# Kernel tuning notes

Hardware: AMD Instinct MI355X
Metric: run time of the kernel (lower is better)

## Reference

```python
import jax, jax.numpy as jnp
import numpy as np

N_PAPER, N_AUTHOR = 200000, 100000
D_PAPER, D_AUTHOR = 128, 64
H, OUT = 64, 32
E_CITES, E_WRITES = 4000000, 2000000


def _gcn(x, W, b, src, dst, n):
    # GCNConv with default add_self_loops=True, symmetric normalization
    xl = x @ W
    deg = jnp.zeros((n,), xl.dtype).at[dst].add(1.0) + 1.0  # +1 for self loop
    dis = jax.lax.rsqrt(deg)
    norm = dis[src] * dis[dst]
    out = jax.ops.segment_sum(xl[src] * norm[:, None], dst, num_segments=n)
    out = out + xl * (dis * dis)[:, None]  # self-loop term: norm_ii = 1/deg_i
    return out + b


def _sage(x_src, x_dst, Wl, bl, Wr, src, dst, n_dst):
    # SAGEConv: mean neighbor aggregation -> lin_l, plus root lin_r on dst
    ones = jnp.ones(src.shape, x_src.dtype)
    cnt = jnp.maximum(jax.ops.segment_sum(ones, dst, num_segments=n_dst), 1.0)
    mean = jax.ops.segment_sum(x_src[src], dst, num_segments=n_dst) / cnt[:, None]
    return mean @ Wl + bl + x_dst @ Wr


def _gat(x_src, x_dst, Ws, Wd, a_s, a_d, b, src, dst, n_dst):
    # GATConv heads=1, bipartite, add_self_loops=False, leaky_relu slope 0.2
    xs = x_src @ Ws  # [Ns, H]
    xd = x_dst @ Wd  # [Nd, H]
    a_src = xs @ a_s  # [Ns]
    a_dst = xd @ a_d  # [Nd]
    e = a_src[src] + a_dst[dst]
    e = jnp.where(e > 0, e, 0.2 * e)
    m = jax.ops.segment_max(e, dst, num_segments=n_dst)
    m = jnp.where(jnp.isfinite(m), m, 0.0)  # nodes with no in-edges
    ex = jnp.exp(e - m[dst])
    denom = jax.ops.segment_sum(ex, dst, num_segments=n_dst)
    alpha = ex / denom[dst]
    out = jax.ops.segment_sum(alpha[:, None] * xs[src], dst, num_segments=n_dst)
    return out + b


def _forward(x_paper, x_author, params, cites_src, cites_dst, writes_src, writes_dst):
    for (gW, gb, sWl, sbl, sWr, aWs, aWd, aas, aad, ab) in params:
        p_gcn = _gcn(x_paper, gW, gb, cites_src, cites_dst, N_PAPER)
        p_sage = _sage(x_author, x_paper, sWl, sbl, sWr, writes_src, writes_dst, N_PAPER)
        # rev_writes: paper -> author, i.e. src=writes_dst (paper), dst=writes_src (author)
        a_gat = _gat(x_paper, x_author, aWs, aWd, aas, aad, ab, writes_dst, writes_src, N_AUTHOR)
        x_paper = jax.nn.relu(p_gcn + p_sage)  # HeteroConv aggr='sum'
        x_author = jax.nn.relu(a_gat)
    return x_paper, x_author


def setup_inputs() -> dict:
    key = jax.random.key(0)
    ks = jax.random.split(key, 40)
    rn = lambda i, shp, s=0.1: jax.random.normal(ks[i], shp, jnp.float32) * s
    inp = {}
    inp['x_paper'] = rn(0, (N_PAPER, D_PAPER), 1.0)
    inp['x_author'] = rn(1, (N_AUTHOR, D_AUTHOR), 1.0)
    dims = [(D_PAPER, D_AUTHOR), (H, H)]
    i = 2
    for l, (dp, da) in enumerate(dims):
        inp[f'gcn_W{l}'] = rn(i, (dp, H)); i += 1
        inp[f'gcn_b{l}'] = jnp.zeros((H,), jnp.float32)
        inp[f'sage_Wl{l}'] = rn(i, (da, H)); i += 1
        inp[f'sage_bl{l}'] = jnp.zeros((H,), jnp.float32)
        inp[f'sage_Wr{l}'] = rn(i, (dp, H)); i += 1
        inp[f'gat_Ws{l}'] = rn(i, (dp, H)); i += 1
        inp[f'gat_Wd{l}'] = rn(i, (da, H)); i += 1
        inp[f'gat_as{l}'] = rn(i, (H,)); i += 1
        inp[f'gat_ad{l}'] = rn(i, (H,)); i += 1
        inp[f'gat_b{l}'] = jnp.zeros((H,), jnp.float32)
    inp['lin_W'] = rn(i, (H, OUT)); i += 1
    inp['lin_b'] = jnp.zeros((OUT,), jnp.float32)
    inp['cites_src'] = jax.random.randint(ks[30], (E_CITES,), 0, N_PAPER)
    inp['cites_dst'] = jax.random.randint(ks[31], (E_CITES,), 0, N_PAPER)
    inp['writes_src'] = jax.random.randint(ks[32], (E_WRITES,), 0, N_AUTHOR)
    inp['writes_dst'] = jax.random.randint(ks[33], (E_WRITES,), 0, N_PAPER)
    return inp


def reference(x_paper, x_author,
              gcn_W0, gcn_b0, sage_Wl0, sage_bl0, sage_Wr0,
              gat_Ws0, gat_Wd0, gat_as0, gat_ad0, gat_b0,
              gcn_W1, gcn_b1, sage_Wl1, sage_bl1, sage_Wr1,
              gat_Ws1, gat_Wd1, gat_as1, gat_ad1, gat_b1,
              lin_W, lin_b,
              cites_src, cites_dst, writes_src, writes_dst):
    params = [
        (gcn_W0, gcn_b0, sage_Wl0, sage_bl0, sage_Wr0, gat_Ws0, gat_Wd0, gat_as0, gat_ad0, gat_b0),
        (gcn_W1, gcn_b1, sage_Wl1, sage_bl1, sage_Wr1, gat_Ws1, gat_Wd1, gat_as1, gat_ad1, gat_b1),
    ]
    _, x_author_out = _forward(x_paper, x_author, params, cites_src, cites_dst, writes_src, writes_dst)
    return x_author_out @ lin_W + lin_b
```

## Files before the change

kernel.cpp:

```cpp
#include <hip/hip_runtime.h>
#include <hip/hip_bf16.h>

#define NP 200000
#define NA 100000
#define DP 128
#define HD 64
#define EC 4000000
#define EW 2000000
#define NSCAN (2 * NP + NA)
#define NBUCK 4
#define CAPC 64
#define CAPW 48
#define CAPA 64

typedef __hip_bfloat16 bf16;
typedef __attribute__((ext_vector_type(8))) short short8;
typedef __attribute__((ext_vector_type(4))) float f32x4;

__device__ __forceinline__ float bf2f(bf16 h) { return __bfloat162float(h); }

__device__ __forceinline__ short8 pack8(float4 a, float4 b) {
    union {
        short8 s;
        unsigned u[4];
    } r;
    __hip_bfloat162 h;
    h = __float22bfloat162_rn(float2{a.x, a.y});
    r.u[0] = *reinterpret_cast<unsigned*>(&h);
    h = __float22bfloat162_rn(float2{a.z, a.w});
    r.u[1] = *reinterpret_cast<unsigned*>(&h);
    h = __float22bfloat162_rn(float2{b.x, b.y});
    r.u[2] = *reinterpret_cast<unsigned*>(&h);
    h = __float22bfloat162_rn(float2{b.z, b.w});
    r.u[3] = *reinterpret_cast<unsigned*>(&h);
    return r.s;
}


__global__ __launch_bounds__(256) void fill_pass_kernel(const int* __restrict__ cs,
                                                        const int* __restrict__ cd,
                                                        const int* __restrict__ ws,
                                                        const int* __restrict__ wd,
                                                        int* __restrict__ CUR,
                                                        int* __restrict__ colC,
                                                        int* __restrict__ colWd,
                                                        int* __restrict__ colWa, int bucket) {
    long i = (long)blockIdx.x * 256 + threadIdx.x;
    if (i < EC) {
        int d = __builtin_nontemporal_load(&cd[i]);
        if ((int)(((long)d * NBUCK) / NP) != bucket) return;
        int s = __builtin_nontemporal_load(&cs[i]);
        int pos = atomicAdd(&CUR[d * 4], 1);
        if (pos < CAPC) colC[(size_t)d * CAPC + pos] = s;
    } else if (i < (long)EC + EW) {
        long e = i - EC;
        int d = __builtin_nontemporal_load(&wd[e]);
        int a = __builtin_nontemporal_load(&ws[e]);
        if ((int)(((long)d * NBUCK) / NP) == bucket) {
            int pos = atomicAdd(&CUR[(NP + d) * 4], 1);
            if (pos < CAPW) colWd[(size_t)d * CAPW + pos] = a;
        }
        if ((int)(((long)a * NBUCK) / NA) == bucket) {
            int pos = atomicAdd(&CUR[(2 * NP + a) * 4], 1);
            if (pos < CAPA) colWa[(size_t)a * CAPA + pos] = d;
        }
    }
}


__global__ __launch_bounds__(256) void conv_author_kernel(const float* __restrict__ XA,
                                                          const float* __restrict__ wvec,
                                                          bf16* __restrict__ XAbf,
                                                          float* __restrict__ adst) {
    __shared__ float vs[64];
    if (threadIdx.x < 64) vs[threadIdx.x] = wvec[threadIdx.x];
    __syncthreads();
    int r = blockIdx.x * 4 + (threadIdx.x >> 6);
    int lane = threadIdx.x & 63;
    float x = XA[(size_t)r * 64 + lane];
    XAbf[(size_t)r * 64 + lane] = __float2bfloat16(x);
    float p = x * vs[lane];
#pragma unroll
    for (int o = 32; o > 0; o >>= 1) p += __shfl_xor(p, o, 64);
    if (lane == 0) adst[r] = p;
}


__global__ void wprep_kernel(const float* __restrict__ Wg, const float* __restrict__ Wl,
                             const float* __restrict__ Wr, const float* __restrict__ Ws0,
                             const float* __restrict__ Ws1, short* __restrict__ WF,
                             const float* __restrict__ Wd0, const float* __restrict__ ad0,
                             const float* __restrict__ Wd1, const float* __restrict__ ad1,
                             float* __restrict__ wvec0, float* __restrict__ wvec1) {
    int bid = blockIdx.x;
    int lane = threadIdx.x;
    if (bid >= 64) {
        const float* Wd = (bid == 64) ? Wd0 : Wd1;
        const float* ad = (bid == 64) ? ad0 : ad1;
        float* wv = (bid == 64) ? wvec0 : wvec1;
        float s = 0.f;
        for (int c = 0; c < 64; c++) s += Wd[lane * 64 + c] * ad[c];
        wv[lane] = s;
        return;
    }
    int q = lane & 15, g = lane >> 4;
    int m, r;
    size_t dst;
    if (bid < 16) {
        m = 0; r = bid; dst = 0;
    } else if (bid < 40) {
        m = 1; r = bid - 16; dst = 8192;
    } else if (bid < 56) {
        m = 2; r = bid - 40; dst = 20480;
    } else {
        m = 3; r = bid - 56; dst = 28672;
    }
    int ks = r >> 2, n = r & 3;
    int col = n * 16 + q;
    float v[8];
#pragma unroll
    for (int j = 0; j < 8; j++) {
        int kr = ks * 32 + g * 8 + j;
        float x;
        if (m == 0) x = Wg[(size_t)kr * 64 + col];
        else if (m == 1) x = (kr < 64) ? Wl[(size_t)kr * 64 + col] : Wr[(size_t)(kr - 64) * 64 + col];
        else if (m == 2) x = Ws0[(size_t)kr * 64 + col];
        else x = Ws1[(size_t)kr * 64 + col];
        v[j] = x;
    }
    short8 s = pack8(float4{v[0], v[1], v[2], v[3]}, float4{v[4], v[5], v[6], v[7]});
    *reinterpret_cast<short8*>(WF + dst + ((size_t)r * 64 + lane) * 8) = s;
}


__global__ __launch_bounds__(256) void fused2_gemm_kernel(const float* __restrict__ XP,
                                                          const short* __restrict__ WFg,
                                                          const short* __restrict__ WFs,
                                                          bf16* __restrict__ BF,
                                                          bf16* __restrict__ XS0,
                                                          const float* __restrict__ avec,
                                                          float* __restrict__ adot,
                                                          const int* __restrict__ CURs) {
    int tid = threadIdx.x;
    int lane = tid & 63, q = lane & 15, g = lane >> 4;
    int rw = blockIdx.x * 64 + (tid >> 6) * 16;
    int arow = rw + q;
    f32x4 accg[4], accs[4];
#pragma unroll
    for (int n = 0; n < 4; n++) {
        accg[n] = f32x4{0.f, 0.f, 0.f, 0.f};
        accs[n] = f32x4{0.f, 0.f, 0.f, 0.f};
    }
#pragma unroll
    for (int ks = 0; ks < 4; ks++) {
        const float* xr = XP + (size_t)arow * DP + ks * 32 + g * 8;
        float4 a0 = *reinterpret_cast<const float4*>(xr);
        float4 a1 = *reinterpret_cast<const float4*>(xr + 4);
        short8 af = pack8(a0, a1);
#pragma unroll
        for (int n = 0; n < 4; n++) {
            short8 bg = *reinterpret_cast<const short8*>(WFg + ((size_t)(ks * 4 + n) * 64 + lane) * 8);
            accg[n] = __builtin_amdgcn_mfma_f32_16x16x32_bf16(af, bg, accg[n], 0, 0, 0);
        }
#pragma unroll
        for (int n = 0; n < 4; n++) {
            short8 bs = *reinterpret_cast<const short8*>(WFs + ((size_t)(ks * 4 + n) * 64 + lane) * 8);
            accs[n] = __builtin_amdgcn_mfma_f32_16x16x32_bf16(af, bs, accs[n], 0, 0, 0);
        }
    }
    float av[4];
#pragma unroll
    for (int n = 0; n < 4; n++) av[n] = avec[n * 16 + q];
#pragma unroll
    for (int j = 0; j < 4; j++) {
        int R = rw + g * 4 + j;
        float sc = rsqrtf((float)CURs[(unsigned)R * 4] + 1.0f);
#pragma unroll
        for (int n = 0; n < 4; n++) {
            BF[(size_t)R * 64 + n * 16 + q] = __float2bfloat16(accg[n][j] * sc);
            XS0[(size_t)R * 64 + n * 16 + q] = __float2bfloat16(accs[n][j]);
        }
        float t = accs[0][j] * av[0] + accs[1][j] * av[1] + accs[2][j] * av[2] + accs[3][j] * av[3];
        t += __shfl_xor(t, 1, 64);
        t += __shfl_xor(t, 2, 64);
        t += __shfl_xor(t, 4, 64);
        t += __shfl_xor(t, 8, 64);
        if (q == 0) adot[R] = t;
    }
}


template <int K, int ASTRIDE, bool ABF16, bool ADOT, bool SCALE>
__global__ __launch_bounds__(256) void mfma_gemm_kernel(const void* __restrict__ Xv,
                                                        const short* __restrict__ Wf,
                                                        bf16* __restrict__ outb,
                                                        const float* __restrict__ avec,
                                                        float* __restrict__ adot,
                                                        const int* __restrict__ CURs) {
    int tid = threadIdx.x;
    int lane = tid & 63, q = lane & 15, g = lane >> 4;
    int rw = blockIdx.x * 64 + (tid >> 6) * 16;
    int arow = rw + q;
    f32x4 acc[4];
#pragma unroll
    for (int n = 0; n < 4; n++) acc[n] = f32x4{0.f, 0.f, 0.f, 0.f};
#pragma unroll
    for (int ks = 0; ks < K / 32; ks++) {
        short8 af;
        if constexpr (ABF16) {
            af = *reinterpret_cast<const short8*>((const bf16*)Xv + (size_t)arow * ASTRIDE +
                                                  ks * 32 + g * 8);
        } else {
            const float* xr = (const float*)Xv + (size_t)arow * ASTRIDE + ks * 32 + g * 8;
            float4 a0 = *reinterpret_cast<const float4*>(xr);
            float4 a1 = *reinterpret_cast<const float4*>(xr + 4);
            af = pack8(a0, a1);
        }
#pragma unroll
        for (int n = 0; n < 4; n++) {
            short8 bfr =
                *reinterpret_cast<const short8*>(Wf + ((size_t)(ks * 4 + n) * 64 + lane) * 8);
            acc[n] = __builtin_amdgcn_mfma_f32_16x16x32_bf16(af, bfr, acc[n], 0, 0, 0);
        }
    }
    float av[4];
    if constexpr (ADOT) {
#pragma unroll
        for (int n = 0; n < 4; n++) av[n] = avec[n * 16 + q];
    }
#pragma unroll
    for (int j = 0; j < 4; j++) {
        int R = rw + g * 4 + j;
        float sc = 1.f;
        if constexpr (SCALE) sc = rsqrtf((float)CURs[(unsigned)R * 4] + 1.0f);
#pragma unroll
        for (int n = 0; n < 4; n++) {
            outb[(size_t)R * 64 + n * 16 + q] = __float2bfloat16(acc[n][j] * sc);
        }
        if constexpr (ADOT) {
            float t = acc[0][j] * av[0] + acc[1][j] * av[1] + acc[2][j] * av[2] + acc[3][j] * av[3];
            t += __shfl_xor(t, 1, 64);
            t += __shfl_xor(t, 2, 64);
            t += __shfl_xor(t, 4, 64);
            t += __shfl_xor(t, 8, 64);
            if (q == 0) adot[R] = t;
        }
    }
}


__global__ __launch_bounds__(256) void mfma_sage_kernel(const bf16* B3s,
                                                        const float* __restrict__ XP,
                                                        const float* __restrict__ B2,
                                                        const float* __restrict__ bl,
                                                        const short* __restrict__ Wf, bf16* P1) {
    int tid = threadIdx.x;
    int lane = tid & 63, q = lane & 15, g = lane >> 4;
    int rw = blockIdx.x * 64 + (tid >> 6) * 16;
    int arow = rw + q;
    f32x4 acc[4];
#pragma unroll
    for (int n = 0; n < 4; n++) acc[n] = f32x4{0.f, 0.f, 0.f, 0.f};
#pragma unroll
    for (int ks = 0; ks < 6; ks++) {
        short8 af;
        if (ks < 2) {
            af = *reinterpret_cast<const short8*>(B3s + (size_t)arow * 128 + 64 + ks * 32 + g * 8);
        } else {
            const float* xr = XP + (size_t)arow * DP + (ks - 2) * 32 + g * 8;
            float4 a0 = *reinterpret_cast<const float4*>(xr);
            float4 a1 = *reinterpret_cast<const float4*>(xr + 4);
            af = pack8(a0, a1);
        }
#pragma unroll
        for (int n = 0; n < 4; n++) {
            short8 bfr =
                *reinterpret_cast<const short8*>(Wf + ((size_t)(ks * 4 + n) * 64 + lane) * 8);
            acc[n] = __builtin_amdgcn_mfma_f32_16x16x32_bf16(af, bfr, acc[n], 0, 0, 0);
        }
    }
    float blv[4];
#pragma unroll
    for (int n = 0; n < 4; n++) blv[n] = bl[n * 16 + q];
#pragma unroll
    for (int j = 0; j < 4; j++) {
        int R = rw + g * 4 + j;
#pragma unroll
        for (int n = 0; n < 4; n++) {
            int col = n * 16 + q;
            float v = acc[n][j] + B2[(size_t)R * 64 + col] + blv[n];
            P1[(size_t)R * 128 + col] = __float2bfloat16(fmaxf(v, 0.f));
        }
    }
}


__global__ __launch_bounds__(256) void paper_gather_kernel(const bf16* __restrict__ B1,
                                                           const bf16* __restrict__ XA,
                                                           const int* __restrict__ CUR,
                                                           const int* colC,
                                                           const int* __restrict__ colWd,
                                                           const float* __restrict__ gb,
                                                           float* __restrict__ B2, bf16* B3s) {
    int node = __builtin_amdgcn_readfirstlane(blockIdx.x * 4 + (threadIdx.x >> 6));
    unsigned lane = threadIdx.x & 63;
    int degc_t = CUR[(unsigned)node * 4];
    float dd = rsqrtf((float)degc_t + 1.0f);
    int degc = min(degc_t, CAPC);
    unsigned cb = (unsigned)node * CAPC;
    float acc = bf2f(B1[((unsigned)node << 6) + lane]);
    int e = 0;
    for (; e + 8 <= degc; e += 8) {
        unsigned off[8];
#pragma unroll
        for (int j = 0; j < 8; j++) off[j] = ((unsigned)colC[cb + e + j] << 6) + lane;
        float v[8];
#pragma unroll
        for (int j = 0; j < 8; j++) v[j] = bf2f(B1[off[j]]);
#pragma unroll
        for (int j = 0; j < 8; j++) acc += v[j];
    }
    for (; e + 4 <= degc; e += 4) {
        unsigned o0 = ((unsigned)colC[cb + e] << 6) + lane;
        unsigned o1 = ((unsigned)colC[cb + e + 1] << 6) + lane;
        unsigned o2 = ((unsigned)colC[cb + e + 2] << 6) + lane;
        unsigned o3 = ((unsigned)colC[cb + e + 3] << 6) + lane;
        float v0 = bf2f(B1[o0]), v1 = bf2f(B1[o1]);
        float v2 = bf2f(B1[o2]), v3 = bf2f(B1[o3]);
        acc += v0 + v1;
        acc += v2 + v3;
    }
    for (; e < degc; e++) acc += bf2f(B1[((unsigned)colC[cb + e] << 6) + lane]);
    B2[((unsigned)node << 6) + lane] = acc * dd + gb[lane];
    int degw_t = CUR[((unsigned)NP + node) * 4];
    float ic = 1.0f / fmaxf((float)degw_t, 1.0f);
    int degw = min(degw_t, CAPW);
    unsigned wb = (unsigned)node * CAPW;
    float s = 0.f;
    e = 0;
    for (; e + 8 <= degw; e += 8) {
        unsigned off[8];
#pragma unroll
        for (int j = 0; j < 8; j++) off[j] = ((unsigned)colWd[wb + e + j] << 6) + lane;
        float v[8];
#pragma unroll
        for (int j = 0; j < 8; j++) v[j] = bf2f(XA[off[j]]);
#pragma unroll
        for (int j = 0; j < 8; j++) s += v[j];
    }
    for (; e + 4 <= degw; e += 4) {
        unsigned o0 = ((unsigned)colWd[wb + e] << 6) + lane;
        unsigned o1 = ((unsigned)colWd[wb + e + 1] << 6) + lane;
        unsigned o2 = ((unsigned)colWd[wb + e + 2] << 6) + lane;
        unsigned o3 = ((unsigned)colWd[wb + e + 3] << 6) + lane;
        float v0 = bf2f(XA[o0]), v1 = bf2f(XA[o1]);
        float v2 = bf2f(XA[o2]), v3 = bf2f(XA[o3]);
        s += v0 + v1;
        s += v2 + v3;
    }
    for (; e < degw; e++) s += bf2f(XA[((unsigned)colWd[wb + e] << 6) + lane]);
    B3s[(unsigned)node * 128u + 64u + lane] = __float2bfloat16(s * ic);
}


__device__ __forceinline__ float lrelu(float v) { return v > 0.f ? v : 0.2f * v; }

__device__ __forceinline__ void gat_phase(const bf16* __restrict__ XS, const int2* pxl, int deg,
                                          unsigned lane, float& accO) {
    float acc = 0.f;
    int l = 0;
    for (; l + 8 <= deg; l += 8) {
        float v[8], x[8];
#pragma unroll
        for (int j = 0; j < 8; j++) {
            int2 px = pxl[l + j];
            x[j] = __int_as_float(px.y);
            v[j] = bf2f(XS[((unsigned)px.x << 6) + lane]);
        }
#pragma unroll
        for (int j = 0; j < 8; j++) acc += x[j] * v[j];
    }
    for (; l < deg; l++) {
        int2 px = pxl[l];
        acc += __int_as_float(px.y) * bf2f(XS[((unsigned)px.x << 6) + lane]);
    }
    accO = acc;
}

__global__ __launch_bounds__(256) void gat_fused_kernel(
    const bf16* __restrict__ XS0, const bf16* __restrict__ XS1, const int* __restrict__ CUR,
    const int* __restrict__ colA, const float* __restrict__ asrc0,
    const float* __restrict__ asrc1, const float* __restrict__ adst0,
    const float* __restrict__ ab0, const float* __restrict__ wvec1,
    const float* __restrict__ ab1, const float* __restrict__ linW,
    const float* __restrict__ linb, float* __restrict__ out) {
    __shared__ float Ws[64 * 32];
    __shared__ float vbuf[4][64];
    __shared__ float lbs[32];
    __shared__ int2 pxlds[4][64];
    int tid = threadIdx.x;
    for (int i = tid; i < 64 * 32; i += 256) Ws[i] = linW[i];
    if (tid < 32) lbs[tid] = linb[tid];
    __syncthreads();
    int wid = tid >> 6;
    int a = __builtin_amdgcn_readfirstlane(blockIdx.x * 4 + wid);
    unsigned lane = tid & 63;
    int deg = min(CUR[(2u * NP + a) * 4], CAPA);
    unsigned cb = (unsigned)a * CAPA;
    int pi = (lane < (unsigned)deg) ? colA[cb + lane] : 0;
    bool act = lane < (unsigned)deg;
    float x0 = act ? __expf(lrelu(asrc0[(unsigned)pi] + adst0[(unsigned)a])) : 0.f;
    float den0 = x0;
#pragma unroll
    for (int o = 32; o > 0; o >>= 1) den0 += __shfl_xor(den0, o, 64);
    pxlds[wid][lane] = int2{pi, __float_as_int(x0)};
    float acc0;
    gat_phase(XS0, pxlds[wid], deg, lane, acc0);
    float inv0 = den0 > 0.f ? 1.f / den0 : 0.f;
    float val0 = fmaxf(acc0 * inv0 + ab0[lane], 0.f);
    float ada1 = val0 * wvec1[lane];
#pragma unroll
    for (int o = 32; o > 0; o >>= 1) ada1 += __shfl_xor(ada1, o, 64);
    float x1 = act ? __expf(lrelu(asrc1[(unsigned)pi] + ada1)) : 0.f;
    float den1 = x1;
#pragma unroll
    for (int o = 32; o > 0; o >>= 1) den1 += __shfl_xor(den1, o, 64);
    pxlds[wid][lane] = int2{pi, __float_as_int(x1)};
    float acc1;
    gat_phase(XS1, pxlds[wid], deg, lane, acc1);
    float inv1 = den1 > 0.f ? 1.f / den1 : 0.f;
    vbuf[wid][lane] = fmaxf(acc1 * inv1 + ab1[lane], 0.f);
    __syncthreads();
    if (tid < 128) {
        int w = tid >> 5, c = tid & 31;
        int node = blockIdx.x * 4 + w;
        float s = lbs[c];
#pragma unroll
        for (int k = 0; k < 64; k++) s += vbuf[w][k] * Ws[k * 32 + c];
        out[(size_t)node * 32 + c] = s;
    }
}


static inline int cdivi(long a, long b) { return (int)((a + b - 1) / b); }

extern "C" void kernel_launch(void* const* d_in, const int* in_sizes, int n_in, void* d_out,
                              int out_size, void* d_ws, size_t ws_size, hipStream_t stream) {
    const float* x_paper = (const float*)d_in[0];
    const float* x_author = (const float*)d_in[1];
    const float* gcn_W0 = (const float*)d_in[2];
    const float* gcn_b0 = (const float*)d_in[3];
    const float* sage_Wl0 = (const float*)d_in[4];
    const float* sage_bl0 = (const float*)d_in[5];
    const float* sage_Wr0 = (const float*)d_in[6];
    const float* gat_Ws0 = (const float*)d_in[7];
    const float* gat_Wd0 = (const float*)d_in[8];
    const float* gat_as0 = (const float*)d_in[9];
    const float* gat_ad0 = (const float*)d_in[10];
    const float* gat_b0 = (const float*)d_in[11];
    const float* gat_Ws1 = (const float*)d_in[17];
    const float* gat_Wd1 = (const float*)d_in[18];
    const float* gat_as1 = (const float*)d_in[19];
    const float* gat_ad1 = (const float*)d_in[20];
    const float* gat_b1 = (const float*)d_in[21];
    const float* lin_W = (const float*)d_in[22];
    const float* lin_b = (const float*)d_in[23];
    const int* cites_src = (const int*)d_in[24];
    const int* cites_dst = (const int*)d_in[25];
    const int* writes_src = (const int*)d_in[26];
    const int* writes_dst = (const int*)d_in[27];

    float* out = (float*)d_out;

    char* base = (char*)d_ws;
    bf16* BF = (bf16*)base;
    base += (size_t)NP * 64 * 2;
    float* B2 = (float*)base;
    base += (size_t)NP * 64 * 4;
    int* colC = (int*)base;
    bf16* R3 = (bf16*)base;
    base += (size_t)NP * CAPC * 4;
    int* colWd = (int*)base;
    bf16* XS1 = (bf16*)base;
    base += (size_t)NP * CAPW * 4;
    int* colWa = (int*)base;
    base += (size_t)NA * CAPA * 4;
    bf16* XAbf = (bf16*)base;
    base += (size_t)NA * 64 * 2;
    bf16* XS0 = (bf16*)base;
    base += (size_t)NP * 64 * 2;
    int* CUR = (int*)base;
    base += (size_t)NSCAN * 4 * 4;
    float* asrc0 = (float*)base;
    float* asrc1 = asrc0 + NP;
    float* adst0 = asrc1 + NP;
    float* wvec0 = adst0 + NA;
    float* wvec1 = wvec0 + 64;
    short* WF = (short*)(wvec1 + 64);

    dim3 blk(256);
    const long EMERGED = (long)EC + EW;

    hipMemsetAsync(CUR, 0, (size_t)NSCAN * 4 * 4, stream);
    wprep_kernel<<<66, 64, 0, stream>>>(gcn_W0, sage_Wl0, sage_Wr0, gat_Ws0, gat_Ws1, WF, gat_Wd0,
                                        gat_ad0, gat_Wd1, gat_ad1, wvec0, wvec1);

    for (int b = 0; b < NBUCK; b++) {
        fill_pass_kernel<<<cdivi(EMERGED, 256), blk, 0, stream>>>(cites_src, cites_dst,
                                                                  writes_src, writes_dst, CUR,
                                                                  colC, colWd, colWa, b);
    }

    conv_author_kernel<<<NA / 4, blk, 0, stream>>>(x_author, wvec0, XAbf, adst0);

    fused2_gemm_kernel<<<NP / 64, blk, 0, stream>>>(x_paper, WF, WF + 20480, BF, XS0, gat_as0,
                                                    asrc0, CUR);

    paper_gather_kernel<<<NP / 4, blk, 0, stream>>>(BF, XAbf, CUR, colC, colWd, gcn_b0, B2, R3);

    mfma_sage_kernel<<<NP / 64, blk, 0, stream>>>(R3, x_paper, B2, sage_bl0, WF + 8192, R3);

    mfma_gemm_kernel<HD, 128, true, true, false><<<NP / 64, blk, 0, stream>>>(
        R3, WF + 28672, XS1, gat_as1, asrc1, nullptr);

    gat_fused_kernel<<<NA / 4, blk, 0, stream>>>(XS0, XS1, CUR, colWa, asrc0, asrc1, adst0,
                                                 gat_b0, wvec1, gat_b1, lin_W, lin_b, out);
}
```

Measured before the change: 792.2 us.

## Fuse SAGE epilogue with layer-1 GAT projection and widen gather unrolls

Merges the SAGE GEMM and the following layer-1 GAT source projection into one kernel. The relu'd paper features stay in LDS and feed a second MFMA, so the intermediate bf16 tensor is never written to or read back from global memory, and one launch is removed. It also adds a 16-wide unrolled edge loop to the paper gather, and makes the GAT phase read its (index, weight) pairs as int4 with 16-wide unrolling to raise memory-level parallelism. The price is higher register pressure and an extra block barrier in the fused kernel.

```diff
diff --git a/kernel.cpp b/kernel.cpp
--- a/kernel.cpp
+++ b/kernel.cpp
@@ -190,73 +190,20 @@
 }
 
 
-template <int K, int ASTRIDE, bool ABF16, bool ADOT, bool SCALE>
-__global__ __launch_bounds__(256) void mfma_gemm_kernel(const void* __restrict__ Xv,
-                                                        const short* __restrict__ Wf,
-                                                        bf16* __restrict__ outb,
-                                                        const float* __restrict__ avec,
-                                                        float* __restrict__ adot,
-                                                        const int* __restrict__ CURs) {
+__global__ __launch_bounds__(256) void sage_l1_kernel(const bf16* __restrict__ B3s,
+                                                      const float* __restrict__ XP,
+                                                      const float* __restrict__ B2,
+                                                      const float* __restrict__ bl,
+                                                      const short* __restrict__ WfS,
+                                                      const short* __restrict__ Wf1,
+                                                      bf16* __restrict__ XS1,
+                                                      const float* __restrict__ avec,
+                                                      float* __restrict__ adot) {
+    __shared__ __align__(16) short Plds[4][16][72];
     int tid = threadIdx.x;
     int lane = tid & 63, q = lane & 15, g = lane >> 4;
-    int rw = blockIdx.x * 64 + (tid >> 6) * 16;
-    int arow = rw + q;
-    f32x4 acc[4];
-#pragma unroll
-    for (int n = 0; n < 4; n++) acc[n] = f32x4{0.f, 0.f, 0.f, 0.f};
-#pragma unroll
-    for (int ks = 0; ks < K / 32; ks++) {
-        short8 af;
-        if constexpr (ABF16) {
-            af = *reinterpret_cast<const short8*>((const bf16*)Xv + (size_t)arow * ASTRIDE +
-                                                  ks * 32 + g * 8);
-        } else {
-            const float* xr = (const float*)Xv + (size_t)arow * ASTRIDE + ks * 32 + g * 8;
-            float4 a0 = *reinterpret_cast<const float4*>(xr);
-            float4 a1 = *reinterpret_cast<const float4*>(xr + 4);
-            af = pack8(a0, a1);
-        }
-#pragma unroll
-        for (int n = 0; n < 4; n++) {
-            short8 bfr =
-                *reinterpret_cast<const short8*>(Wf + ((size_t)(ks * 4 + n) * 64 + lane) * 8);
-            acc[n] = __builtin_amdgcn_mfma_f32_16x16x32_bf16(af, bfr, acc[n], 0, 0, 0);
-        }
-    }
-    float av[4];
-    if constexpr (ADOT) {
-#pragma unroll
-        for (int n = 0; n < 4; n++) av[n] = avec[n * 16 + q];
-    }
-#pragma unroll
-    for (int j = 0; j < 4; j++) {
-        int R = rw + g * 4 + j;
-        float sc = 1.f;
-        if constexpr (SCALE) sc = rsqrtf((float)CURs[(unsigned)R * 4] + 1.0f);
-#pragma unroll
-        for (int n = 0; n < 4; n++) {
-            outb[(size_t)R * 64 + n * 16 + q] = __float2bfloat16(acc[n][j] * sc);
-        }
-        if constexpr (ADOT) {
-            float t = acc[0][j] * av[0] + acc[1][j] * av[1] + acc[2][j] * av[2] + acc[3][j] * av[3];
-            t += __shfl_xor(t, 1, 64);
-            t += __shfl_xor(t, 2, 64);
-            t += __shfl_xor(t, 4, 64);
-            t += __shfl_xor(t, 8, 64);
-            if (q == 0) adot[R] = t;
-        }
-    }
-}
-
-
-__global__ __launch_bounds__(256) void mfma_sage_kernel(const bf16* B3s,
-                                                        const float* __restrict__ XP,
-                                                        const float* __restrict__ B2,
-                                                        const float* __restrict__ bl,
-                                                        const short* __restrict__ Wf, bf16* P1) {
-    int tid = threadIdx.x;
-    int lane = tid & 63, q = lane & 15, g = lane >> 4;
-    int rw = blockIdx.x * 64 + (tid >> 6) * 16;
+    int wv = tid >> 6;
+    int rw = blockIdx.x * 64 + wv * 16;
     int arow = rw + q;
     f32x4 acc[4];
 #pragma unroll
@@ -275,7 +222,7 @@
 #pragma unroll
         for (int n = 0; n < 4; n++) {
             short8 bfr =
-                *reinterpret_cast<const short8*>(Wf + ((size_t)(ks * 4 + n) * 64 + lane) * 8);
+                *reinterpret_cast<const short8*>(WfS + ((size_t)(ks * 4 + n) * 64 + lane) * 8);
             acc[n] = __builtin_amdgcn_mfma_f32_16x16x32_bf16(af, bfr, acc[n], 0, 0, 0);
         }
     }
@@ -289,8 +236,40 @@
         for (int n = 0; n < 4; n++) {
             int col = n * 16 + q;
             float v = acc[n][j] + B2[(size_t)R * 64 + col] + blv[n];
-            P1[(size_t)R * 128 + col] = __float2bfloat16(fmaxf(v, 0.f));
-        }
+            bf16 h = __float2bfloat16(fmaxf(v, 0.f));
+            Plds[wv][g * 4 + j][col] = *reinterpret_cast<short*>(&h);
+        }
+    }
+    __syncthreads();
+    f32x4 acc2[4];
+#pragma unroll
+    for (int n = 0; n < 4; n++) acc2[n] = f32x4{0.f, 0.f, 0.f, 0.f};
+#pragma unroll
+    for (int ks = 0; ks < 2; ks++) {
+        short8 af = *reinterpret_cast<const short8*>(&Plds[wv][q][ks * 32 + g * 8]);
+#pragma unroll
+        for (int n = 0; n < 4; n++) {
+            short8 bfr =
+                *reinterpret_cast<const short8*>(Wf1 + ((size_t)(ks * 4 + n) * 64 + lane) * 8);
+            acc2[n] = __builtin_amdgcn_mfma_f32_16x16x32_bf16(af, bfr, acc2[n], 0, 0, 0);
+        }
+    }
+    float av[4];
+#pragma unroll
+    for (int n = 0; n < 4; n++) av[n] = avec[n * 16 + q];
+#pragma unroll
+    for (int j = 0; j < 4; j++) {
+        int R = rw + g * 4 + j;
+#pragma unroll
+        for (int n = 0; n < 4; n++) {
+            XS1[(size_t)R * 64 + n * 16 + q] = __float2bfloat16(acc2[n][j]);
+        }
+        float t = acc2[0][j] * av[0] + acc2[1][j] * av[1] + acc2[2][j] * av[2] + acc2[3][j] * av[3];
+        t += __shfl_xor(t, 1, 64);
+        t += __shfl_xor(t, 2, 64);
+        t += __shfl_xor(t, 4, 64);
+        t += __shfl_xor(t, 8, 64);
+        if (q == 0) adot[R] = t;
     }
 }
 
@@ -310,6 +289,16 @@
     unsigned cb = (unsigned)node * CAPC;
     float acc = bf2f(B1[((unsigned)node << 6) + lane]);
     int e = 0;
+    for (; e + 16 <= degc; e += 16) {
+        unsigned off[16];
+#pragma unroll
+        for (int j = 0; j < 16; j++) off[j] = ((unsigned)colC[cb + e + j] << 6) + lane;
+        float v[16];
+#pragma unroll
+        for (int j = 0; j < 16; j++) v[j] = bf2f(B1[off[j]]);
+#pragma unroll
+        for (int j = 0; j < 16; j++) acc += v[j];
+    }
     for (; e + 8 <= degc; e += 8) {
         unsigned off[8];
 #pragma unroll
@@ -367,18 +356,40 @@
 
 __device__ __forceinline__ void gat_phase(const bf16* __restrict__ XS, const int2* pxl, int deg,
                                           unsigned lane, float& accO) {
+    const int4* px4 = reinterpret_cast<const int4*>(pxl);
     float acc = 0.f;
     int l = 0;
+    for (; l + 16 <= deg; l += 16) {
+        int4 pp[8];
+#pragma unroll
+        for (int j = 0; j < 8; j++) pp[j] = px4[(l >> 1) + j];
+        float v[16];
+#pragma unroll
+        for (int j = 0; j < 8; j++) {
+            v[2 * j] = bf2f(XS[((unsigned)pp[j].x << 6) + lane]);
+            v[2 * j + 1] = bf2f(XS[((unsigned)pp[j].z << 6) + lane]);
+        }
+#pragma unroll
+        for (int j = 0; j < 8; j++) {
+            acc += __int_as_float(pp[j].y) * v[2 * j];
+            acc += __int_as_float(pp[j].w) * v[2 * j + 1];
+        }
+    }
     for (; l + 8 <= deg; l += 8) {
-        float v[8], x[8];
-#pragma unroll
-        for (int j = 0; j < 8; j++) {
-            int2 px = pxl[l + j];
-            x[j] = __int_as_float(px.y);
-            v[j] = bf2f(XS[((unsigned)px.x << 6) + lane]);
-        }
-#pragma unroll
-        for (int j = 0; j < 8; j++) acc += x[j] * v[j];
+        int4 pp[4];
+#pragma unroll
+        for (int j = 0; j < 4; j++) pp[j] = px4[(l >> 1) + j];
+        float v[8];
+#pragma unroll
+        for (int j = 0; j < 4; j++) {
+            v[2 * j] = bf2f(XS[((unsigned)pp[j].x << 6) + lane]);
+            v[2 * j + 1] = bf2f(XS[((unsigned)pp[j].z << 6) + lane]);
+        }
+#pragma unroll
+        for (int j = 0; j < 4; j++) {
+            acc += __int_as_float(pp[j].y) * v[2 * j];
+            acc += __int_as_float(pp[j].w) * v[2 * j + 1];
+        }
     }
     for (; l < deg; l++) {
         int2 px = pxl[l];
@@ -397,7 +408,7 @@
     __shared__ float Ws[64 * 32];
     __shared__ float vbuf[4][64];
     __shared__ float lbs[32];
-    __shared__ int2 pxlds[4][64];
+    __shared__ __align__(16) int2 pxlds[4][64];
     int tid = threadIdx.x;
     for (int i = tid; i < 64 * 32; i += 256) Ws[i] = linW[i];
     if (tid < 32) lbs[tid] = linb[tid];
@@ -518,10 +529,8 @@
 
     paper_gather_kernel<<<NP / 4, blk, 0, stream>>>(BF, XAbf, CUR, colC, colWd, gcn_b0, B2, R3);
 
-    mfma_sage_kernel<<<NP / 64, blk, 0, stream>>>(R3, x_paper, B2, sage_bl0, WF + 8192, R3);
-
-    mfma_gemm_kernel<HD, 128, true, true, false><<<NP / 64, blk, 0, stream>>>(
-        R3, WF + 28672, XS1, gat_as1, asrc1, nullptr);
+    sage_l1_kernel<<<NP / 64, blk, 0, stream>>>(R3, x_paper, B2, sage_bl0, WF + 8192, WF + 28672,
+                                                XS1, gat_as1, asrc1);
 
     gat_fused_kernel<<<NA / 4, blk, 0, stream>>>(XS0, XS1, CUR, colWa, asrc0, asrc1, adst0,
                                                  gat_b0, wvec1, gat_b1, lin_W, lin_b, out);
```

New measurement: 789.9 us. About the same (-0.3%).
